# Optimization experiments

Hardware: AMD Instinct MI355X
Metric: run time of the kernel (lower is better)

The kernel has to match this reference:

```python
import jax, jax.numpy as jnp
import numpy as np

N_NODES = 100000

def _sage(x, src, tgt, Wl, bl, Wr):
    # PyG SAGEConv (mean aggr): out = lin_l(mean_{j in N(i)} x_j) + lin_r(x_i)
    msg = x[src]                                             # [E, F] gather
    s = jax.ops.segment_sum(msg, tgt, num_segments=N_NODES)  # [N, F]
    cnt = jax.ops.segment_sum(jnp.ones((src.shape[0], 1), x.dtype), tgt, num_segments=N_NODES)
    agg = s / jnp.maximum(cnt, 1.0)
    return agg @ Wl + bl + x @ Wr


def setup_inputs() -> dict:
    key = jax.random.key(0)
    ks = jax.random.split(key, 16)
    node_dim, edge_dim, hidden = 128, 16, 64
    E = 1000000
    x = jax.random.normal(ks[0], (N_NODES, node_dim), jnp.float32)
    edge_index = jax.random.randint(ks[1], (2, E), 0, N_NODES, jnp.int64)
    edge_attr = jax.random.normal(ks[2], (E, edge_dim), jnp.float32)
    def lin(k, fi, fo, scale=None):
        s = scale if scale is not None else 1.0 / np.sqrt(fi)
        return jax.random.uniform(k, (fi, fo), jnp.float32, -s, s)
    return {
        "x": x, "edge_index": edge_index, "edge_attr": edge_attr,
        # edge MLP: Linear(16,64) -> ReLU -> Linear(64,64)
        "We1": lin(ks[3], edge_dim, hidden), "be1": jnp.zeros((hidden,), jnp.float32),
        "We2": lin(ks[4], hidden, hidden),   "be2": jnp.zeros((hidden,), jnp.float32),
        # SAGEConv 0: lin_l (with bias, on aggregated) + lin_r (no bias, on root)
        "Wl0": lin(ks[5], node_dim, hidden), "bl0": jnp.zeros((hidden,), jnp.float32),
        "Wr0": lin(ks[6], node_dim, hidden),
        # SAGEConv 1
        "Wl1": lin(ks[7], hidden, hidden), "bl1": jnp.zeros((hidden,), jnp.float32),
        "Wr1": lin(ks[8], hidden, hidden),
        # output MLP: Linear(64,64) -> ReLU -> (Dropout eval=id) -> Linear(64,1)
        "Wo1": lin(ks[9], hidden, hidden), "bo1": jnp.zeros((hidden,), jnp.float32),
        "Wo2": lin(ks[10], hidden, 1),     "bo2": jnp.zeros((1,), jnp.float32),
    }


def reference(x, edge_index, edge_attr, We1, be1, We2, be2,
              Wl0, bl0, Wr0, Wl1, bl1, Wr1, Wo1, bo1, Wo2, bo2):
    src, tgt = edge_index[0], edge_index[1]
    # edge MLP (dropout in eval mode = identity)
    ea = jax.nn.relu(edge_attr @ We1 + be1) @ We2 + be2       # [E, H]
    # two SAGE layers with ReLU
    h = jax.nn.relu(_sage(x, src, tgt, Wl0, bl0, Wr0))        # [N, H]
    h = jax.nn.relu(_sage(h, src, tgt, Wl1, bl1, Wr1))        # [N, H]
    # per-edge features: gather both endpoints + edge embedding
    ef = h[src] + h[tgt] + ea                                 # [E, H]
    out = jax.nn.relu(ef @ Wo1 + bo1) @ Wo2 + bo2             # [E, 1]
    return jax.nn.sigmoid(out[:, 0])                          # [E]
```

## Files before the change

kernel.cpp:

```cpp
#include <hip/hip_runtime.h>
#include <math.h>

typedef __attribute__((ext_vector_type(8))) short short8;
typedef __attribute__((ext_vector_type(4))) float f32x4;

static __device__ __forceinline__ unsigned short f2bf(float f) {
  union { float f; unsigned int u; } x; x.f = f;
  unsigned int r = x.u + 0x7fffu + ((x.u >> 16) & 1u);
  return (unsigned short)(r >> 16);
}
static __device__ __forceinline__ float bf2f(unsigned int u) {
  union { unsigned int u; float f; } x; x.u = u << 16; return x.f;
}

__global__ void k_flag(const unsigned int* __restrict__ w, int nSample,
                       unsigned int* __restrict__ flag,
                       int* __restrict__ deg, int padN) {
  int4* d4 = (int4*)deg;
  int n4 = padN >> 2;
  for (int i = blockIdx.x * 256 + threadIdx.x; i < n4; i += gridDim.x * 256)
    d4[i] = make_int4(0, 0, 0, 0);
  if (blockIdx.x != 0) return;
  __shared__ unsigned int red[256];
  unsigned int v = 0;
  for (int i = threadIdx.x; i < nSample; i += 256) v |= w[2 * i + 1];
  red[threadIdx.x] = v;
  __syncthreads();
  for (int s = 128; s > 0; s >>= 1) {
    if (threadIdx.x < s) red[threadIdx.x] |= red[threadIdx.x + s];
    __syncthreads();
  }
  if (threadIdx.x == 0) flag[0] = red[0];
}

__global__ void k_decode(const unsigned int* __restrict__ w,
                         const unsigned int* __restrict__ flag, int E,
                         const float4* __restrict__ ef,
                         uint2* __restrict__ eb,
                         int* __restrict__ src, int* __restrict__ tgt,
                         int* __restrict__ posin, int* __restrict__ deg) {
  int gid = blockIdx.x * 256 + threadIdx.x;
  int stride = gridDim.x * 256;
  for (int i = gid; i < E * 4; i += stride) {
    float4 v = ef[i];
    uint2 pk;
    pk.x = (unsigned int)f2bf(v.x) | ((unsigned int)f2bf(v.y) << 16);
    pk.y = (unsigned int)f2bf(v.z) | ((unsigned int)f2bf(v.w) << 16);
    eb[i] = pk;
  }
  int e = gid;
  if (e >= E) return;
  int s, t;
  if (flag[0]) { s = (int)w[e]; t = (int)w[E + e]; }
  else         { s = (int)w[2 * e]; t = (int)w[2 * (E + e)]; }
  src[e] = s;
  tgt[e] = t;
  posin[e] = atomicAdd(deg + t, 1);
}

__global__ __launch_bounds__(256) void k_scan1(const int* __restrict__ deg,
                                               int* __restrict__ bsum) {
  __shared__ int wsum[4];
  const int tid = threadIdx.x, lane = tid & 63, wid = tid >> 6;
  const int base = blockIdx.x * 2048 + tid * 8;
  int4 v0 = *(const int4*)(deg + base);
  int4 v1 = *(const int4*)(deg + base + 4);
  int s = v0.x + v0.y + v0.z + v0.w + v1.x + v1.y + v1.z + v1.w;
#pragma unroll
  for (int off = 1; off < 64; off <<= 1) s += __shfl_xor(s, off, 64);
  if (lane == 0) wsum[wid] = s;
  __syncthreads();
  if (tid == 0) bsum[blockIdx.x] = wsum[0] + wsum[1] + wsum[2] + wsum[3];
}

__global__ void k_scan2(const int* __restrict__ bsum, int* __restrict__ boff,
                        int nB) {
  int lane = threadIdx.x;
  int v = (lane < nB) ? bsum[lane] : 0;
  int incl = v;
#pragma unroll
  for (int off = 1; off < 64; off <<= 1) {
    int t = __shfl_up(incl, off, 64);
    if (lane >= off) incl += t;
  }
  if (lane < nB) boff[lane] = incl - v;
}

__global__ __launch_bounds__(256) void k_scan3(const int* __restrict__ deg,
                                               const int* __restrict__ boff,
                                               int* __restrict__ rowptr) {
  __shared__ int wsum[4];
  const int tid = threadIdx.x, lane = tid & 63, wid = tid >> 6;
  const int base = blockIdx.x * 2048 + tid * 8;
  int4 v0 = *(const int4*)(deg + base);
  int4 v1 = *(const int4*)(deg + base + 4);
  int e[8] = {v0.x, v0.y, v0.z, v0.w, v1.x, v1.y, v1.z, v1.w};
  int s = e[0] + e[1] + e[2] + e[3] + e[4] + e[5] + e[6] + e[7];
  int incl = s;
#pragma unroll
  for (int off = 1; off < 64; off <<= 1) {
    int t = __shfl_up(incl, off, 64);
    if (lane >= off) incl += t;
  }
  if (lane == 63) wsum[wid] = incl;
  __syncthreads();
  int run = boff[blockIdx.x] + (incl - s);
  for (int w = 0; w < wid; ++w) run += wsum[w];
  int o[8];
#pragma unroll
  for (int i = 0; i < 8; ++i) { o[i] = run; run += e[i]; }
  *(int4*)(rowptr + base) = make_int4(o[0], o[1], o[2], o[3]);
  *(int4*)(rowptr + base + 4) = make_int4(o[4], o[5], o[6], o[7]);
}

__global__ void k_fill(const int* __restrict__ src, const int* __restrict__ tgt,
                       const int* __restrict__ posin,
                       const int* __restrict__ rowptr,
                       int* __restrict__ csrc, int E) {
  int e = blockIdx.x * 256 + threadIdx.x;
  if (e >= E) return;
  csrc[rowptr[tgt[e]] + posin[e]] = src[e];
}

__global__ __launch_bounds__(256) void k_prepall(
    const float* __restrict__ We2, const float* __restrict__ Wo1,
    const float* __restrict__ be2, const float* __restrict__ bo1,
    const float* __restrict__ We1,
    const float* __restrict__ Wl0, const float* __restrict__ Wr0,
    const float* __restrict__ Wl1, const float* __restrict__ Wr1,
    unsigned short* __restrict__ W25T, unsigned short* __restrict__ We1T,
    unsigned short* __restrict__ Wo1T, float* __restrict__ cvec,
    unsigned short* __restrict__ WnT0, unsigned short* __restrict__ WnT1) {
  const int tid = threadIdx.x;
  if (blockIdx.x == 0) {
    __shared__ float sA[4096];
    __shared__ float sB[4096];
    for (int i = tid; i < 1024; i += 256) {
      *(float4*)&sA[i * 4] = *(const float4*)(We2 + i * 4);
      *(float4*)&sB[i * 4] = *(const float4*)(Wo1 + i * 4);
    }
    __syncthreads();
    for (int idx = tid; idx < 4096; idx += 256) {
      int n = idx >> 6, k = idx & 63;
      float s = 0.f;
#pragma unroll 8
      for (int mm = 0; mm < 64; ++mm) s = fmaf(sA[k * 64 + mm], sB[mm * 64 + n], s);
      W25T[idx] = f2bf(s);
      Wo1T[idx] = f2bf(sB[k * 64 + n]);
    }
    for (int idx = tid; idx < 2048; idx += 256) {
      int n = idx >> 5, k = idx & 31;
      We1T[n * 32 + k] = (k < 16) ? f2bf(We1[k * 64 + n]) : (unsigned short)0;
    }
    if (tid < 64) {
      float s = bo1[tid];
#pragma unroll 8
      for (int mm = 0; mm < 64; ++mm) s = fmaf(be2[mm], sB[mm * 64 + tid], s);
      cvec[tid] = s;
    }
  } else if (blockIdx.x <= 64) {
    int idx = (blockIdx.x - 1) * 256 + tid;
    int n = idx >> 7, k = idx & 127;
    float v = (n < 64) ? Wl0[(size_t)k * 64 + n] : Wr0[(size_t)k * 64 + (n - 64)];
    WnT0[idx] = f2bf(v);
  } else {
    int idx = (blockIdx.x - 65) * 256 + tid;
    int n = idx >> 6, k = idx & 63;
    float v = (n < 64) ? Wl1[(size_t)k * 64 + n] : Wr1[(size_t)k * 64 + (n - 64)];
    WnT1[idx] = f2bf(v);
  }
}

template <int K, bool BF16IN, int NTILES>
__global__ __launch_bounds__(256) void k_ngemm(
    const void* __restrict__ Xv, const unsigned short* __restrict__ WnT,
    unsigned short* __restrict__ Y0, unsigned short* __restrict__ Y1, int N) {
  constexpr int STR = K + 8;
  constexpr int NC = K / 32;
  __shared__ unsigned short sX[64 * STR];
  const int tid = threadIdx.x;
  const int wv = tid >> 6, lane = tid & 63;
  const int m = lane & 15, q = lane >> 4;
  const int row0 = blockIdx.x * 64;

  short8 bB[NTILES][NC];
#pragma unroll
  for (int ct = 0; ct < NTILES; ++ct)
#pragma unroll
    for (int c = 0; c < NC; ++c) {
      int n = (NTILES == 2) ? (wv * 32 + ct * 16 + m) : (wv * 16 + m);
      bB[ct][c] = *(const short8*)(WnT + (size_t)n * K + c * 32 + q * 8);
    }

#pragma unroll
  for (int i = 0; i < K / 16; ++i) {
    int f = tid + 256 * i;
    int r = f / (K / 4);
    int c4 = f % (K / 4);
    int rr = row0 + r; if (rr >= N) rr = N - 1;
    uint2 pk;
    if constexpr (BF16IN) {
      pk = *(const uint2*)((const unsigned short*)Xv + (size_t)rr * K + c4 * 4);
    } else {
      float4 v = *(const float4*)((const float*)Xv + (size_t)rr * K + c4 * 4);
      pk.x = (unsigned int)f2bf(v.x) | ((unsigned int)f2bf(v.y) << 16);
      pk.y = (unsigned int)f2bf(v.z) | ((unsigned int)f2bf(v.w) << 16);
    }
    *(uint2*)(sX + r * STR + c4 * 4) = pk;
  }
  __syncthreads();

  f32x4 acc[4][NTILES];
#pragma unroll
  for (int rt = 0; rt < 4; ++rt)
#pragma unroll
    for (int ct = 0; ct < NTILES; ++ct)
#pragma unroll
      for (int r = 0; r < 4; ++r) acc[rt][ct][r] = 0.f;

#pragma unroll
  for (int c = 0; c < NC; ++c) {
    short8 a[4];
#pragma unroll
    for (int rt = 0; rt < 4; ++rt)
      a[rt] = *(const short8*)(sX + (rt * 16 + m) * STR + c * 32 + q * 8);
#pragma unroll
    for (int rt = 0; rt < 4; ++rt)
#pragma unroll
      for (int ct = 0; ct < NTILES; ++ct)
        acc[rt][ct] = __builtin_amdgcn_mfma_f32_16x16x32_bf16(a[rt], bB[ct][c], acc[rt][ct], 0, 0, 0);
  }

#pragma unroll
  for (int rt = 0; rt < 4; ++rt)
#pragma unroll
    for (int ct = 0; ct < NTILES; ++ct) {
      unsigned short* Yw;
      int n;
      if constexpr (NTILES == 2) {
        Yw = (wv < 2) ? Y0 : Y1;
        n = (wv & 1) * 32 + ct * 16 + m;
      } else {
        Yw = Y0;
        n = wv * 16 + m;
      }
#pragma unroll
      for (int reg = 0; reg < 4; ++reg) {
        int row = row0 + rt * 16 + q * 4 + reg;
        if (row < N) Yw[(size_t)row * 64 + n] = f2bf(acc[rt][ct][reg]);
      }
    }
}

__global__ __launch_bounds__(256) void k_agg(
    const unsigned short* __restrict__ Y, const int* __restrict__ rowptr,
    const int* __restrict__ csrc, const float* __restrict__ bias,
    const unsigned short* __restrict__ Yr, unsigned short* __restrict__ H,
    int N) {
  int node = (blockIdx.x * 256 + threadIdx.x) >> 6;
  if (node >= N) return;
  const int lane = threadIdx.x & 63;
  const int c4 = lane & 15, rr = lane >> 4;
  int beg = rowptr[node], end = rowptr[node + 1];
  float a0 = 0.f, a1 = 0.f, a2 = 0.f, a3 = 0.f;
  float b0 = 0.f, b1 = 0.f, b2 = 0.f, b3 = 0.f;
  for (int e = beg; e < end; e += 8) {
    int e0 = e + rr, e1 = e + 4 + rr;
    if (e0 < end) {
      int s = csrc[e0];
      uint2 v = *(const uint2*)(Y + (size_t)s * 64 + c4 * 4);
      a0 += bf2f(v.x & 0xffffu); a1 += bf2f(v.x >> 16);
      a2 += bf2f(v.y & 0xffffu); a3 += bf2f(v.y >> 16);
    }
    if (e1 < end) {
      int s = csrc[e1];
      uint2 v = *(const uint2*)(Y + (size_t)s * 64 + c4 * 4);
      b0 += bf2f(v.x & 0xffffu); b1 += bf2f(v.x >> 16);
      b2 += bf2f(v.y & 0xffffu); b3 += bf2f(v.y >> 16);
    }
  }
  a0 += b0; a1 += b1; a2 += b2; a3 += b3;
#pragma unroll
  for (int msk = 16; msk <= 32; msk <<= 1) {
    a0 += __shfl_xor(a0, msk, 64);
    a1 += __shfl_xor(a1, msk, 64);
    a2 += __shfl_xor(a2, msk, 64);
    a3 += __shfl_xor(a3, msk, 64);
  }
  if (rr == 0) {
    float cdeg = (float)(end - beg);
    if (cdeg < 1.f) cdeg = 1.f;
    float inv = 1.f / cdeg;
    float4 bv = *(const float4*)(bias + c4 * 4);
    uint2 yv = *(const uint2*)(Yr + (size_t)node * 64 + c4 * 4);
    float o0 = fmaxf(a0 * inv + bv.x + bf2f(yv.x & 0xffffu), 0.f);
    float o1 = fmaxf(a1 * inv + bv.y + bf2f(yv.x >> 16), 0.f);
    float o2 = fmaxf(a2 * inv + bv.z + bf2f(yv.y & 0xffffu), 0.f);
    float o3 = fmaxf(a3 * inv + bv.w + bf2f(yv.y >> 16), 0.f);
    uint2 pk;
    pk.x = (unsigned int)f2bf(o0) | ((unsigned int)f2bf(o1) << 16);
    pk.y = (unsigned int)f2bf(o2) | ((unsigned int)f2bf(o3) << 16);
    *(uint2*)(H + (size_t)node * 64 + c4 * 4) = pk;
  }
}

#define T1_STRIDE 72
#define G_STRIDE 68
__global__ __launch_bounds__(256) void k_edge3(
    const unsigned short* __restrict__ EAb, const int* __restrict__ src,
    const int* __restrict__ tgt, const unsigned short* __restrict__ Gb,
    const unsigned short* __restrict__ We1T,
    const unsigned short* __restrict__ W25T,
    const float* __restrict__ cvec, const float* __restrict__ be1,
    const float* __restrict__ Wo2, const float* __restrict__ bo2,
    float* __restrict__ out, int E, int nT, int nWaves) {
  __shared__ unsigned short sT1a[4][16 * T1_STRIDE];
  __shared__ float sGa[4][16 * G_STRIDE];
  const int tid = threadIdx.x;
  const int wid = tid >> 6, lane = tid & 63;
  const int m = lane & 15, q = lane >> 4;
  unsigned short* sT1 = sT1a[wid];
  float* sG = sGa[wid];

  short8 bWe1[4], bW25[4][2];
  float cv[4], wo2v[4], be1v[4];
#pragma unroll
  for (int nt = 0; nt < 4; ++nt) {
    int n = nt * 16 + m;
    bWe1[nt] = *(const short8*)(We1T + n * 32 + q * 8);
    bW25[nt][0] = *(const short8*)(W25T + n * 64 + q * 8);
    bW25[nt][1] = *(const short8*)(W25T + n * 64 + 32 + q * 8);
    cv[nt] = cvec[n];
    wo2v[nt] = Wo2[n];
    be1v[nt] = be1[n];
  }
  const float b_out = bo2[0];
  const short8 zfrag = {};

  int t = blockIdx.x * 4 + wid;
  if (t >= nT) return;
  int il = t * 16 + m; if (il >= E) il = E - 1;
  int my_idx = (lane < 16) ? src[il] : ((lane < 32) ? tgt[il] : 0);

  while (true) {
    const int base = t * 16;
    const int tn = t + nWaves;
    const bool last = (tn >= nT);
    const int tc = last ? t : tn;

    int il_n = tc * 16 + m; if (il_n >= E) il_n = E - 1;
    int idx_n = (lane < 16) ? src[il_n] : ((lane < 32) ? tgt[il_n] : 0);

    int rs[4], rt[4];
#pragma unroll
    for (int r = 0; r < 4; ++r) {
      rs[r] = __shfl(my_idx, q * 4 + r, 64);
      rt[r] = __shfl(my_idx, 16 + q * 4 + r, 64);
    }
    uint2 sv[4], tv[4];
#pragma unroll
    for (int r = 0; r < 4; ++r) {
      sv[r] = *(const uint2*)(Gb + (size_t)rs[r] * 64 + m * 4);
      tv[r] = *(const uint2*)(Gb + (size_t)rt[r] * 64 + m * 4);
    }

    int er = base + m; if (er >= E) er = E - 1;
    short8 aEA = zfrag;
    if (q < 2) aEA = *(const short8*)(EAb + (size_t)er * 16 + (q & 1) * 8);

    f32x4 t1[4];
#pragma unroll
    for (int nt = 0; nt < 4; ++nt) {
      f32x4 cinit; cinit[0] = be1v[nt]; cinit[1] = be1v[nt];
      cinit[2] = be1v[nt]; cinit[3] = be1v[nt];
      t1[nt] = __builtin_amdgcn_mfma_f32_16x16x32_bf16(aEA, bWe1[nt], cinit, 0, 0, 0);
    }
#pragma unroll
    for (int nt = 0; nt < 4; ++nt)
#pragma unroll
      for (int r = 0; r < 4; ++r)
        sT1[(q * 4 + r) * T1_STRIDE + nt * 16 + m] = f2bf(fmaxf(t1[nt][r], 0.f));
    short8 aT0 = *(short8*)(sT1 + m * T1_STRIDE + q * 8);
    short8 aT1 = *(short8*)(sT1 + m * T1_STRIDE + 32 + q * 8);

#pragma unroll
    for (int r = 0; r < 4; ++r) {
      f32x4 g;
      g[0] = bf2f(sv[r].x & 0xffffu) + bf2f(tv[r].x & 0xffffu);
      g[1] = bf2f(sv[r].x >> 16)     + bf2f(tv[r].x >> 16);
      g[2] = bf2f(sv[r].y & 0xffffu) + bf2f(tv[r].y & 0xffffu);
      g[3] = bf2f(sv[r].y >> 16)     + bf2f(tv[r].y >> 16);
      *(f32x4*)(sG + (q * 4 + r) * G_STRIDE + m * 4) = g;
    }

    f32x4 acc[4];
#pragma unroll
    for (int nt = 0; nt < 4; ++nt)
#pragma unroll
      for (int r = 0; r < 4; ++r)
        acc[nt][r] = cv[nt] + sG[(q * 4 + r) * G_STRIDE + nt * 16 + m];
#pragma unroll
    for (int nt = 0; nt < 4; ++nt) {
      acc[nt] = __builtin_amdgcn_mfma_f32_16x16x32_bf16(aT0, bW25[nt][0], acc[nt], 0, 0, 0);
      acc[nt] = __builtin_amdgcn_mfma_f32_16x16x32_bf16(aT1, bW25[nt][1], acc[nt], 0, 0, 0);
    }

    float p[4];
#pragma unroll
    for (int r = 0; r < 4; ++r) {
      p[r] = fmaxf(acc[0][r], 0.f) * wo2v[0] + fmaxf(acc[1][r], 0.f) * wo2v[1] +
             fmaxf(acc[2][r], 0.f) * wo2v[2] + fmaxf(acc[3][r], 0.f) * wo2v[3];
    }
#pragma unroll
    for (int msk = 1; msk <= 8; msk <<= 1) {
#pragma unroll
      for (int r = 0; r < 4; ++r) p[r] += __shfl_xor(p[r], msk, 64);
    }
    if (m == 0) {
#pragma unroll
      for (int r = 0; r < 4; ++r) {
        int row = base + q * 4 + r;
        if (row < E) out[row] = 1.f / (1.f + __expf(-(p[r] + b_out)));
      }
    }

    if (last) break;
    t = tn; my_idx = idx_n;
  }
}

extern "C" void kernel_launch(void* const* d_in, const int* in_sizes, int n_in,
                              void* d_out, int out_size, void* d_ws, size_t ws_size,
                              hipStream_t stream) {
  const float* x     = (const float*)d_in[0];
  const unsigned int* eidx = (const unsigned int*)d_in[1];
  const float* eattr = (const float*)d_in[2];
  const float* We1 = (const float*)d_in[3];
  const float* be1 = (const float*)d_in[4];
  const float* We2 = (const float*)d_in[5];
  const float* be2 = (const float*)d_in[6];
  const float* Wl0 = (const float*)d_in[7];
  const float* bl0 = (const float*)d_in[8];
  const float* Wr0 = (const float*)d_in[9];
  const float* Wl1 = (const float*)d_in[10];
  const float* bl1 = (const float*)d_in[11];
  const float* Wr1 = (const float*)d_in[12];
  const float* Wo1 = (const float*)d_in[13];
  const float* bo1 = (const float*)d_in[14];
  const float* Wo2 = (const float*)d_in[15];
  const float* bo2 = (const float*)d_in[16];

  const int N = in_sizes[0] / 128;
  const int E = in_sizes[2] / 16;
  const int padN = (N + 2047) & ~2047;
  const int nB = padN / 2048;
  float* out = (float*)d_out;

  char* ws = (char*)d_ws;
  size_t off = 0;
  auto alloc = [&](size_t bytes) {
    char* p = ws + off;
    off += (bytes + 255) & ~(size_t)255;
    return p;
  };
  unsigned int* flag = (unsigned int*)alloc(256);
  int* src    = (int*)alloc((size_t)E * 4);
  int* tgt    = (int*)alloc((size_t)E * 4);
  int* posin  = (int*)alloc((size_t)E * 4);
  int* deg    = (int*)alloc((size_t)padN * 4);
  int* rowptr = (int*)alloc((size_t)(padN + 64) * 4);
  int* bsum   = (int*)alloc(64 * 4);
  int* boff   = (int*)alloc(64 * 4);
  int* csrc   = (int*)alloc((size_t)E * 4);
  unsigned short* EAb = (unsigned short*)alloc((size_t)E * 16 * 2);
  unsigned short* Hb = (unsigned short*)alloc((size_t)N * 64 * 2);
  unsigned short* Yl = (unsigned short*)alloc((size_t)N * 64 * 2);
  unsigned short* Yr = (unsigned short*)alloc((size_t)N * 64 * 2);
  unsigned short* Gb = (unsigned short*)alloc((size_t)N * 64 * 2);
  unsigned short* W25T = (unsigned short*)alloc(64 * 64 * 2);
  unsigned short* We1T = (unsigned short*)alloc(64 * 32 * 2);
  unsigned short* Wo1T = (unsigned short*)alloc(64 * 64 * 2);
  unsigned short* WnT0 = (unsigned short*)alloc(128 * 128 * 2);
  unsigned short* WnT1 = (unsigned short*)alloc(128 * 64 * 2);
  float* cvec = (float*)alloc(64 * 4);
  (void)ws_size; (void)n_in; (void)out_size;

  k_flag<<<64, 256, 0, stream>>>(eidx, 8192, flag, deg, padN);
  k_decode<<<(E + 255) / 256, 256, 0, stream>>>(
      eidx, flag, E, (const float4*)eattr, (uint2*)EAb, src, tgt, posin, deg);
  k_scan1<<<nB, 256, 0, stream>>>(deg, bsum);
  k_scan2<<<1, 64, 0, stream>>>(bsum, boff, nB);
  k_scan3<<<nB, 256, 0, stream>>>(deg, boff, rowptr);
  k_fill<<<(E + 255) / 256, 256, 0, stream>>>(src, tgt, posin, rowptr, csrc, E);
  k_prepall<<<97, 256, 0, stream>>>(We2, Wo1, be2, bo1, We1, Wl0, Wr0, Wl1, Wr1,
                                    W25T, We1T, Wo1T, cvec, WnT0, WnT1);

  const int gB = (N + 63) / 64;
  k_ngemm<128, false, 2><<<gB, 256, 0, stream>>>(x, WnT0, Yl, Yr, N);
  k_agg<<<(N + 3) / 4, 256, 0, stream>>>(Yl, rowptr, csrc, bl0, Yr, Hb, N);

  k_ngemm<64, true, 2><<<gB, 256, 0, stream>>>(Hb, WnT1, Yl, Yr, N);
  k_agg<<<(N + 3) / 4, 256, 0, stream>>>(Yl, rowptr, csrc, bl1, Yr, Hb, N);

  k_ngemm<64, true, 1><<<gB, 256, 0, stream>>>(Hb, Wo1T, Gb, nullptr, N);

  const int nT = (E + 15) / 16;
  const int blocks = 3072;
  k_edge3<<<blocks, 256, 0, stream>>>(EAb, src, tgt, Gb, We1T, W25T, cvec,
                                      be1, Wo2, bo2, out, E, nT, blocks * 4);
}
```

Baseline: 456.4 us.

## Merge independent launches into horizontally fused multi-role kernels

Independent stages now share a launch through block-index role dispatch. Edge decoding is merged with weight preparation, the CSR fill with the first node GEMM, and the edge-attribute bf16 conversion with the first aggregation. This removes several kernel launches and lets bandwidth-bound and gather-bound work overlap on the GPU. The W25T prep now reads We2 from global memory instead of shared memory. Mixed roles inside one grid can unbalance scheduling, and the fused kernels may use more registers or LDS.

```diff
diff --git a/kernel.cpp b/kernel.cpp
--- a/kernel.cpp
+++ b/kernel.cpp
@@ -33,29 +33,66 @@
   if (threadIdx.x == 0) flag[0] = red[0];
 }
 
-__global__ void k_decode(const unsigned int* __restrict__ w,
-                         const unsigned int* __restrict__ flag, int E,
-                         const float4* __restrict__ ef,
-                         uint2* __restrict__ eb,
-                         int* __restrict__ src, int* __restrict__ tgt,
-                         int* __restrict__ posin, int* __restrict__ deg) {
-  int gid = blockIdx.x * 256 + threadIdx.x;
-  int stride = gridDim.x * 256;
-  for (int i = gid; i < E * 4; i += stride) {
-    float4 v = ef[i];
-    uint2 pk;
-    pk.x = (unsigned int)f2bf(v.x) | ((unsigned int)f2bf(v.y) << 16);
-    pk.y = (unsigned int)f2bf(v.z) | ((unsigned int)f2bf(v.w) << 16);
-    eb[i] = pk;
-  }
-  int e = gid;
-  if (e >= E) return;
-  int s, t;
-  if (flag[0]) { s = (int)w[e]; t = (int)w[E + e]; }
-  else         { s = (int)w[2 * e]; t = (int)w[2 * (E + e)]; }
-  src[e] = s;
-  tgt[e] = t;
-  posin[e] = atomicAdd(deg + t, 1);
+__global__ __launch_bounds__(256) void k_mega1(
+    const unsigned int* __restrict__ w, const unsigned int* __restrict__ flag,
+    int E, int nDec,
+    int* __restrict__ src, int* __restrict__ tgt,
+    int* __restrict__ posin, int* __restrict__ deg,
+    const float* __restrict__ We2, const float* __restrict__ Wo1,
+    const float* __restrict__ be2, const float* __restrict__ bo1,
+    const float* __restrict__ We1,
+    const float* __restrict__ Wl0, const float* __restrict__ Wr0,
+    const float* __restrict__ Wl1, const float* __restrict__ Wr1,
+    unsigned short* __restrict__ W25T, unsigned short* __restrict__ We1T,
+    unsigned short* __restrict__ Wo1T, float* __restrict__ cvec,
+    unsigned short* __restrict__ WnT0, unsigned short* __restrict__ WnT1) {
+  __shared__ float sB[4096];
+  const int tid = threadIdx.x;
+  if (blockIdx.x < nDec) {
+    int e = blockIdx.x * 256 + tid;
+    if (e >= E) return;
+    int s, t;
+    if (flag[0]) { s = (int)w[e]; t = (int)w[E + e]; }
+    else         { s = (int)w[2 * e]; t = (int)w[2 * (E + e)]; }
+    src[e] = s;
+    tgt[e] = t;
+    posin[e] = atomicAdd(deg + t, 1);
+    return;
+  }
+  const int b = blockIdx.x - nDec;
+  if (b == 0) {
+    for (int i = tid; i < 1024; i += 256)
+      *(float4*)&sB[i * 4] = *(const float4*)(Wo1 + i * 4);
+    __syncthreads();
+    for (int idx = tid; idx < 4096; idx += 256) {
+      int k = idx >> 6, n = idx & 63;
+      float s = 0.f;
+#pragma unroll 8
+      for (int mm = 0; mm < 64; ++mm) s = fmaf(We2[k * 64 + mm], sB[mm * 64 + n], s);
+      W25T[n * 64 + k] = f2bf(s);
+      Wo1T[n * 64 + k] = f2bf(sB[k * 64 + n]);
+    }
+    for (int idx = tid; idx < 2048; idx += 256) {
+      int n = idx >> 5, k = idx & 31;
+      We1T[n * 32 + k] = (k < 16) ? f2bf(We1[k * 64 + n]) : (unsigned short)0;
+    }
+    if (tid < 64) {
+      float s = bo1[tid];
+#pragma unroll 8
+      for (int mm = 0; mm < 64; ++mm) s = fmaf(be2[mm], sB[mm * 64 + tid], s);
+      cvec[tid] = s;
+    }
+  } else if (b <= 64) {
+    int idx = (b - 1) * 256 + tid;
+    int n = idx >> 7, k = idx & 127;
+    float v = (n < 64) ? Wl0[(size_t)k * 64 + n] : Wr0[(size_t)k * 64 + (n - 64)];
+    WnT0[idx] = f2bf(v);
+  } else {
+    int idx = (b - 65) * 256 + tid;
+    int n = idx >> 6, k = idx & 63;
+    float v = (n < 64) ? Wl1[(size_t)k * 64 + n] : Wr1[(size_t)k * 64 + (n - 64)];
+    WnT1[idx] = f2bf(v);
+  }
 }
 
 __global__ __launch_bounds__(256) void k_scan1(const int* __restrict__ deg,
@@ -113,75 +150,18 @@
   *(int4*)(rowptr + base + 4) = make_int4(o[4], o[5], o[6], o[7]);
 }
 
-__global__ void k_fill(const int* __restrict__ src, const int* __restrict__ tgt,
-                       const int* __restrict__ posin,
-                       const int* __restrict__ rowptr,
-                       int* __restrict__ csrc, int E) {
-  int e = blockIdx.x * 256 + threadIdx.x;
-  if (e >= E) return;
-  csrc[rowptr[tgt[e]] + posin[e]] = src[e];
-}
-
-__global__ __launch_bounds__(256) void k_prepall(
-    const float* __restrict__ We2, const float* __restrict__ Wo1,
-    const float* __restrict__ be2, const float* __restrict__ bo1,
-    const float* __restrict__ We1,
-    const float* __restrict__ Wl0, const float* __restrict__ Wr0,
-    const float* __restrict__ Wl1, const float* __restrict__ Wr1,
-    unsigned short* __restrict__ W25T, unsigned short* __restrict__ We1T,
-    unsigned short* __restrict__ Wo1T, float* __restrict__ cvec,
-    unsigned short* __restrict__ WnT0, unsigned short* __restrict__ WnT1) {
-  const int tid = threadIdx.x;
-  if (blockIdx.x == 0) {
-    __shared__ float sA[4096];
-    __shared__ float sB[4096];
-    for (int i = tid; i < 1024; i += 256) {
-      *(float4*)&sA[i * 4] = *(const float4*)(We2 + i * 4);
-      *(float4*)&sB[i * 4] = *(const float4*)(Wo1 + i * 4);
-    }
-    __syncthreads();
-    for (int idx = tid; idx < 4096; idx += 256) {
-      int n = idx >> 6, k = idx & 63;
-      float s = 0.f;
-#pragma unroll 8
-      for (int mm = 0; mm < 64; ++mm) s = fmaf(sA[k * 64 + mm], sB[mm * 64 + n], s);
-      W25T[idx] = f2bf(s);
-      Wo1T[idx] = f2bf(sB[k * 64 + n]);
-    }
-    for (int idx = tid; idx < 2048; idx += 256) {
-      int n = idx >> 5, k = idx & 31;
-      We1T[n * 32 + k] = (k < 16) ? f2bf(We1[k * 64 + n]) : (unsigned short)0;
-    }
-    if (tid < 64) {
-      float s = bo1[tid];
-#pragma unroll 8
-      for (int mm = 0; mm < 64; ++mm) s = fmaf(be2[mm], sB[mm * 64 + tid], s);
-      cvec[tid] = s;
-    }
-  } else if (blockIdx.x <= 64) {
-    int idx = (blockIdx.x - 1) * 256 + tid;
-    int n = idx >> 7, k = idx & 127;
-    float v = (n < 64) ? Wl0[(size_t)k * 64 + n] : Wr0[(size_t)k * 64 + (n - 64)];
-    WnT0[idx] = f2bf(v);
-  } else {
-    int idx = (blockIdx.x - 65) * 256 + tid;
-    int n = idx >> 6, k = idx & 63;
-    float v = (n < 64) ? Wl1[(size_t)k * 64 + n] : Wr1[(size_t)k * 64 + (n - 64)];
-    WnT1[idx] = f2bf(v);
-  }
-}
-
 template <int K, bool BF16IN, int NTILES>
-__global__ __launch_bounds__(256) void k_ngemm(
+__device__ __forceinline__ void ngemm_body(
     const void* __restrict__ Xv, const unsigned short* __restrict__ WnT,
-    unsigned short* __restrict__ Y0, unsigned short* __restrict__ Y1, int N) {
+    unsigned short* __restrict__ Y0, unsigned short* __restrict__ Y1,
+    int N, int blk) {
   constexpr int STR = K + 8;
   constexpr int NC = K / 32;
   __shared__ unsigned short sX[64 * STR];
   const int tid = threadIdx.x;
   const int wv = tid >> 6, lane = tid & 63;
   const int m = lane & 15, q = lane >> 4;
-  const int row0 = blockIdx.x * 64;
+  const int row0 = blk * 64;
 
   short8 bB[NTILES][NC];
 #pragma unroll
@@ -252,12 +232,35 @@
     }
 }
 
-__global__ __launch_bounds__(256) void k_agg(
+template <int K, bool BF16IN, int NTILES>
+__global__ __launch_bounds__(256) void k_ngemm(
+    const void* __restrict__ Xv, const unsigned short* __restrict__ WnT,
+    unsigned short* __restrict__ Y0, unsigned short* __restrict__ Y1, int N) {
+  ngemm_body<K, BF16IN, NTILES>(Xv, WnT, Y0, Y1, N, blockIdx.x);
+}
+
+__global__ __launch_bounds__(256) void k_mega2(
+    const void* __restrict__ Xv, const unsigned short* __restrict__ WnT,
+    unsigned short* __restrict__ Y0, unsigned short* __restrict__ Y1, int N,
+    int gB,
+    const int* __restrict__ src, const int* __restrict__ tgt,
+    const int* __restrict__ posin, const int* __restrict__ rowptr,
+    int* __restrict__ csrc, int E) {
+  if (blockIdx.x < gB) {
+    ngemm_body<128, false, 2>(Xv, WnT, Y0, Y1, N, blockIdx.x);
+  } else {
+    int e = (blockIdx.x - gB) * 256 + threadIdx.x;
+    if (e >= E) return;
+    csrc[rowptr[tgt[e]] + posin[e]] = src[e];
+  }
+}
+
+__device__ __forceinline__ void agg_body(
     const unsigned short* __restrict__ Y, const int* __restrict__ rowptr,
     const int* __restrict__ csrc, const float* __restrict__ bias,
     const unsigned short* __restrict__ Yr, unsigned short* __restrict__ H,
-    int N) {
-  int node = (blockIdx.x * 256 + threadIdx.x) >> 6;
+    int N, int blk) {
+  int node = (blk * 256 + threadIdx.x) >> 6;
   if (node >= N) return;
   const int lane = threadIdx.x & 63;
   const int c4 = lane & 15, rr = lane >> 4;
@@ -301,6 +304,35 @@
     pk.x = (unsigned int)f2bf(o0) | ((unsigned int)f2bf(o1) << 16);
     pk.y = (unsigned int)f2bf(o2) | ((unsigned int)f2bf(o3) << 16);
     *(uint2*)(H + (size_t)node * 64 + c4 * 4) = pk;
+  }
+}
+
+__global__ __launch_bounds__(256) void k_agg(
+    const unsigned short* __restrict__ Y, const int* __restrict__ rowptr,
+    const int* __restrict__ csrc, const float* __restrict__ bias,
+    const unsigned short* __restrict__ Yr, unsigned short* __restrict__ H,
+    int N) {
+  agg_body(Y, rowptr, csrc, bias, Yr, H, N, blockIdx.x);
+}
+
+__global__ __launch_bounds__(256) void k_aggc(
+    const unsigned short* __restrict__ Y, const int* __restrict__ rowptr,
+    const int* __restrict__ csrc, const float* __restrict__ bias,
+    const unsigned short* __restrict__ Yr, unsigned short* __restrict__ H,
+    int N, int aggB,
+    const float4* __restrict__ ef, uint2* __restrict__ eb, int nItems,
+    int nConvThreads) {
+  if (blockIdx.x < aggB) {
+    agg_body(Y, rowptr, csrc, bias, Yr, H, N, blockIdx.x);
+  } else {
+    int gid = (blockIdx.x - aggB) * 256 + threadIdx.x;
+    for (int i = gid; i < nItems; i += nConvThreads) {
+      float4 v = ef[i];
+      uint2 pk;
+      pk.x = (unsigned int)f2bf(v.x) | ((unsigned int)f2bf(v.y) << 16);
+      pk.y = (unsigned int)f2bf(v.z) | ((unsigned int)f2bf(v.w) << 16);
+      eb[i] = pk;
+    }
   }
 }
 
@@ -486,21 +518,29 @@
   (void)ws_size; (void)n_in; (void)out_size;
 
   k_flag<<<64, 256, 0, stream>>>(eidx, 8192, flag, deg, padN);
-  k_decode<<<(E + 255) / 256, 256, 0, stream>>>(
-      eidx, flag, E, (const float4*)eattr, (uint2*)EAb, src, tgt, posin, deg);
+
+  const int nDec = (E + 255) / 256;
+  k_mega1<<<nDec + 97, 256, 0, stream>>>(
+      eidx, flag, E, nDec, src, tgt, posin, deg,
+      We2, Wo1, be2, bo1, We1, Wl0, Wr0, Wl1, Wr1,
+      W25T, We1T, Wo1T, cvec, WnT0, WnT1);
+
   k_scan1<<<nB, 256, 0, stream>>>(deg, bsum);
   k_scan2<<<1, 64, 0, stream>>>(bsum, boff, nB);
   k_scan3<<<nB, 256, 0, stream>>>(deg, boff, rowptr);
-  k_fill<<<(E + 255) / 256, 256, 0, stream>>>(src, tgt, posin, rowptr, csrc, E);
-  k_prepall<<<97, 256, 0, stream>>>(We2, Wo1, be2, bo1, We1, Wl0, Wr0, Wl1, Wr1,
-                                    W25T, We1T, Wo1T, cvec, WnT0, WnT1);
 
   const int gB = (N + 63) / 64;
-  k_ngemm<128, false, 2><<<gB, 256, 0, stream>>>(x, WnT0, Yl, Yr, N);
-  k_agg<<<(N + 3) / 4, 256, 0, stream>>>(Yl, rowptr, csrc, bl0, Yr, Hb, N);
+  k_mega2<<<gB + nDec, 256, 0, stream>>>(x, WnT0, Yl, Yr, N, gB,
+                                         src, tgt, posin, rowptr, csrc, E);
+
+  const int aggB = (N + 3) / 4;
+  const int convB = 2048;
+  k_aggc<<<aggB + convB, 256, 0, stream>>>(Yl, rowptr, csrc, bl0, Yr, Hb, N,
+                                           aggB, (const float4*)eattr,
+                                           (uint2*)EAb, E * 4, convB * 256);
 
   k_ngemm<64, true, 2><<<gB, 256, 0, stream>>>(Hb, WnT1, Yl, Yr, N);
-  k_agg<<<(N + 3) / 4, 256, 0, stream>>>(Yl, rowptr, csrc, bl1, Yr, Hb, N);
+  k_agg<<<aggB, 256, 0, stream>>>(Yl, rowptr, csrc, bl1, Yr, Hb, N);
 
   k_ngemm<64, true, 1><<<gB, 256, 0, stream>>>(Hb, Wo1T, Gb, nullptr, N);
 
```

After: 446.2 us. 1.02x faster.

## Fuse edge decode, weight prep, first node GEMM and edge-attr conversion into one kernel

Applied to the files above, without the earlier changes.

Merges edge index decoding with degree atomics, weight transposition and packing, the first-layer node GEMM, and the edge-attribute bf16 conversion into a single heterogeneous launch. Block roles are interleaved so decode blocks are spread among the work blocks. The first GEMM now reads fp32 weights directly and converts them inline, which drops the separate prep kernel and the WnT0 buffer. This removes several launches and their serialization so independent memory-bound work can overlap, at the cost of redundant per-block weight conversion and a bulkier kernel with shared-memory sizing tied to the largest role.

```diff
diff --git a/kernel.cpp b/kernel.cpp
--- a/kernel.cpp
+++ b/kernel.cpp
@@ -33,163 +33,37 @@
   if (threadIdx.x == 0) flag[0] = red[0];
 }
 
-__global__ void k_decode(const unsigned int* __restrict__ w,
-                         const unsigned int* __restrict__ flag, int E,
-                         const float4* __restrict__ ef,
-                         uint2* __restrict__ eb,
-                         int* __restrict__ src, int* __restrict__ tgt,
-                         int* __restrict__ posin, int* __restrict__ deg) {
-  int gid = blockIdx.x * 256 + threadIdx.x;
-  int stride = gridDim.x * 256;
-  for (int i = gid; i < E * 4; i += stride) {
-    float4 v = ef[i];
-    uint2 pk;
-    pk.x = (unsigned int)f2bf(v.x) | ((unsigned int)f2bf(v.y) << 16);
-    pk.y = (unsigned int)f2bf(v.z) | ((unsigned int)f2bf(v.w) << 16);
-    eb[i] = pk;
-  }
-  int e = gid;
-  if (e >= E) return;
-  int s, t;
-  if (flag[0]) { s = (int)w[e]; t = (int)w[E + e]; }
-  else         { s = (int)w[2 * e]; t = (int)w[2 * (E + e)]; }
-  src[e] = s;
-  tgt[e] = t;
-  posin[e] = atomicAdd(deg + t, 1);
-}
-
-__global__ __launch_bounds__(256) void k_scan1(const int* __restrict__ deg,
-                                               int* __restrict__ bsum) {
-  __shared__ int wsum[4];
-  const int tid = threadIdx.x, lane = tid & 63, wid = tid >> 6;
-  const int base = blockIdx.x * 2048 + tid * 8;
-  int4 v0 = *(const int4*)(deg + base);
-  int4 v1 = *(const int4*)(deg + base + 4);
-  int s = v0.x + v0.y + v0.z + v0.w + v1.x + v1.y + v1.z + v1.w;
-#pragma unroll
-  for (int off = 1; off < 64; off <<= 1) s += __shfl_xor(s, off, 64);
-  if (lane == 0) wsum[wid] = s;
-  __syncthreads();
-  if (tid == 0) bsum[blockIdx.x] = wsum[0] + wsum[1] + wsum[2] + wsum[3];
-}
-
-__global__ void k_scan2(const int* __restrict__ bsum, int* __restrict__ boff,
-                        int nB) {
-  int lane = threadIdx.x;
-  int v = (lane < nB) ? bsum[lane] : 0;
-  int incl = v;
-#pragma unroll
-  for (int off = 1; off < 64; off <<= 1) {
-    int t = __shfl_up(incl, off, 64);
-    if (lane >= off) incl += t;
-  }
-  if (lane < nB) boff[lane] = incl - v;
-}
-
-__global__ __launch_bounds__(256) void k_scan3(const int* __restrict__ deg,
-                                               const int* __restrict__ boff,
-                                               int* __restrict__ rowptr) {
-  __shared__ int wsum[4];
-  const int tid = threadIdx.x, lane = tid & 63, wid = tid >> 6;
-  const int base = blockIdx.x * 2048 + tid * 8;
-  int4 v0 = *(const int4*)(deg + base);
-  int4 v1 = *(const int4*)(deg + base + 4);
-  int e[8] = {v0.x, v0.y, v0.z, v0.w, v1.x, v1.y, v1.z, v1.w};
-  int s = e[0] + e[1] + e[2] + e[3] + e[4] + e[5] + e[6] + e[7];
-  int incl = s;
-#pragma unroll
-  for (int off = 1; off < 64; off <<= 1) {
-    int t = __shfl_up(incl, off, 64);
-    if (lane >= off) incl += t;
-  }
-  if (lane == 63) wsum[wid] = incl;
-  __syncthreads();
-  int run = boff[blockIdx.x] + (incl - s);
-  for (int w = 0; w < wid; ++w) run += wsum[w];
-  int o[8];
-#pragma unroll
-  for (int i = 0; i < 8; ++i) { o[i] = run; run += e[i]; }
-  *(int4*)(rowptr + base) = make_int4(o[0], o[1], o[2], o[3]);
-  *(int4*)(rowptr + base + 4) = make_int4(o[4], o[5], o[6], o[7]);
-}
-
-__global__ void k_fill(const int* __restrict__ src, const int* __restrict__ tgt,
-                       const int* __restrict__ posin,
-                       const int* __restrict__ rowptr,
-                       int* __restrict__ csrc, int E) {
-  int e = blockIdx.x * 256 + threadIdx.x;
-  if (e >= E) return;
-  csrc[rowptr[tgt[e]] + posin[e]] = src[e];
-}
-
-__global__ __launch_bounds__(256) void k_prepall(
-    const float* __restrict__ We2, const float* __restrict__ Wo1,
-    const float* __restrict__ be2, const float* __restrict__ bo1,
-    const float* __restrict__ We1,
-    const float* __restrict__ Wl0, const float* __restrict__ Wr0,
-    const float* __restrict__ Wl1, const float* __restrict__ Wr1,
-    unsigned short* __restrict__ W25T, unsigned short* __restrict__ We1T,
-    unsigned short* __restrict__ Wo1T, float* __restrict__ cvec,
-    unsigned short* __restrict__ WnT0, unsigned short* __restrict__ WnT1) {
-  const int tid = threadIdx.x;
-  if (blockIdx.x == 0) {
-    __shared__ float sA[4096];
-    __shared__ float sB[4096];
-    for (int i = tid; i < 1024; i += 256) {
-      *(float4*)&sA[i * 4] = *(const float4*)(We2 + i * 4);
-      *(float4*)&sB[i * 4] = *(const float4*)(Wo1 + i * 4);
-    }
-    __syncthreads();
-    for (int idx = tid; idx < 4096; idx += 256) {
-      int n = idx >> 6, k = idx & 63;
-      float s = 0.f;
-#pragma unroll 8
-      for (int mm = 0; mm < 64; ++mm) s = fmaf(sA[k * 64 + mm], sB[mm * 64 + n], s);
-      W25T[idx] = f2bf(s);
-      Wo1T[idx] = f2bf(sB[k * 64 + n]);
-    }
-    for (int idx = tid; idx < 2048; idx += 256) {
-      int n = idx >> 5, k = idx & 31;
-      We1T[n * 32 + k] = (k < 16) ? f2bf(We1[k * 64 + n]) : (unsigned short)0;
-    }
-    if (tid < 64) {
-      float s = bo1[tid];
-#pragma unroll 8
-      for (int mm = 0; mm < 64; ++mm) s = fmaf(be2[mm], sB[mm * 64 + tid], s);
-      cvec[tid] = s;
-    }
-  } else if (blockIdx.x <= 64) {
-    int idx = (blockIdx.x - 1) * 256 + tid;
-    int n = idx >> 7, k = idx & 127;
-    float v = (n < 64) ? Wl0[(size_t)k * 64 + n] : Wr0[(size_t)k * 64 + (n - 64)];
-    WnT0[idx] = f2bf(v);
-  } else {
-    int idx = (blockIdx.x - 65) * 256 + tid;
-    int n = idx >> 6, k = idx & 63;
-    float v = (n < 64) ? Wl1[(size_t)k * 64 + n] : Wr1[(size_t)k * 64 + (n - 64)];
-    WnT1[idx] = f2bf(v);
-  }
-}
-
-template <int K, bool BF16IN, int NTILES>
-__global__ __launch_bounds__(256) void k_ngemm(
+template <int K, bool BF16IN, int NTILES, bool INLINEW>
+__device__ __forceinline__ void ngemm_body(
     const void* __restrict__ Xv, const unsigned short* __restrict__ WnT,
-    unsigned short* __restrict__ Y0, unsigned short* __restrict__ Y1, int N) {
+    const float* __restrict__ W0f, const float* __restrict__ W1f,
+    unsigned short* __restrict__ Y0, unsigned short* __restrict__ Y1,
+    int N, int blk, unsigned short* __restrict__ sX) {
   constexpr int STR = K + 8;
   constexpr int NC = K / 32;
-  __shared__ unsigned short sX[64 * STR];
   const int tid = threadIdx.x;
   const int wv = tid >> 6, lane = tid & 63;
   const int m = lane & 15, q = lane >> 4;
-  const int row0 = blockIdx.x * 64;
+  const int row0 = blk * 64;
 
   short8 bB[NTILES][NC];
 #pragma unroll
   for (int ct = 0; ct < NTILES; ++ct)
 #pragma unroll
     for (int c = 0; c < NC; ++c) {
-      int n = (NTILES == 2) ? (wv * 32 + ct * 16 + m) : (wv * 16 + m);
-      bB[ct][c] = *(const short8*)(WnT + (size_t)n * K + c * 32 + q * 8);
+      if constexpr (INLINEW) {
+        int n = (NTILES == 2) ? (wv * 32 + ct * 16 + m) : (wv * 16 + m);
+        const float* Wf = (n < 64) ? W0f : W1f;
+        int nn = n & 63;
+        union { short8 s; unsigned short h[8]; } ub;
+#pragma unroll
+        for (int j = 0; j < 8; ++j)
+          ub.h[j] = f2bf(Wf[(size_t)(c * 32 + q * 8 + j) * 64 + nn]);
+        bB[ct][c] = ub.s;
+      } else {
+        int n = (NTILES == 2) ? (wv * 32 + ct * 16 + m) : (wv * 16 + m);
+        bB[ct][c] = *(const short8*)(WnT + (size_t)n * K + c * 32 + q * 8);
+      }
     }
 
 #pragma unroll
@@ -250,6 +124,157 @@
         if (row < N) Yw[(size_t)row * 64 + n] = f2bf(acc[rt][ct][reg]);
       }
     }
+}
+
+template <int K, bool BF16IN, int NTILES>
+__global__ __launch_bounds__(256) void k_ngemm(
+    const void* __restrict__ Xv, const unsigned short* __restrict__ WnT,
+    unsigned short* __restrict__ Y0, unsigned short* __restrict__ Y1, int N) {
+  __shared__ __align__(16) unsigned short sX[64 * (K + 8)];
+  ngemm_body<K, BF16IN, NTILES, false>(Xv, WnT, nullptr, nullptr, Y0, Y1, N,
+                                       blockIdx.x, sX);
+}
+
+__global__ __launch_bounds__(256) void k_mega1(
+    const unsigned int* __restrict__ w, const unsigned int* __restrict__ flag,
+    int E, int nDec, int nWork, int gB, int nConvThreads,
+    int* __restrict__ src, int* __restrict__ tgt,
+    int* __restrict__ posin, int* __restrict__ deg,
+    const float* __restrict__ x, unsigned short* __restrict__ Yl,
+    unsigned short* __restrict__ Yr, int N,
+    const float* __restrict__ We2, const float* __restrict__ Wo1,
+    const float* __restrict__ be2, const float* __restrict__ bo1,
+    const float* __restrict__ We1,
+    const float* __restrict__ Wl0, const float* __restrict__ Wr0,
+    const float* __restrict__ Wl1, const float* __restrict__ Wr1,
+    unsigned short* __restrict__ W25T, unsigned short* __restrict__ We1T,
+    unsigned short* __restrict__ Wo1T, float* __restrict__ cvec,
+    unsigned short* __restrict__ WnT1,
+    const float4* __restrict__ ef, uint2* __restrict__ eb) {
+  __shared__ __align__(16) char smem[64 * 136 * 2];
+  const int tid = threadIdx.x;
+  const int tot = nDec + nWork;
+  const int di  = (int)(((long long)blockIdx.x * nDec) / tot);
+  const int di1 = (int)(((long long)(blockIdx.x + 1) * nDec) / tot);
+
+  if (di1 > di) {
+    int e = di * 256 + tid;
+    if (e >= E) return;
+    int s, t;
+    if (flag[0]) { s = (int)w[e]; t = (int)w[E + e]; }
+    else         { s = (int)w[2 * e]; t = (int)w[2 * (E + e)]; }
+    src[e] = s;
+    tgt[e] = t;
+    posin[e] = atomicAdd(deg + t, 1);
+    return;
+  }
+  const int wi = blockIdx.x - di;
+  if (wi == 0) {
+    float* sB = (float*)smem;
+    for (int i = tid; i < 1024; i += 256)
+      *(float4*)&sB[i * 4] = *(const float4*)(Wo1 + i * 4);
+    __syncthreads();
+    for (int idx = tid; idx < 4096; idx += 256) {
+      int k = idx >> 6, n = idx & 63;
+      float s = 0.f;
+#pragma unroll 8
+      for (int mm = 0; mm < 64; ++mm) s = fmaf(We2[k * 64 + mm], sB[mm * 64 + n], s);
+      W25T[n * 64 + k] = f2bf(s);
+      Wo1T[n * 64 + k] = f2bf(sB[k * 64 + n]);
+    }
+    for (int idx = tid; idx < 2048; idx += 256) {
+      int n = idx >> 5, k = idx & 31;
+      We1T[n * 32 + k] = (k < 16) ? f2bf(We1[k * 64 + n]) : (unsigned short)0;
+    }
+    if (tid < 64) {
+      float s = bo1[tid];
+#pragma unroll 8
+      for (int mm = 0; mm < 64; ++mm) s = fmaf(be2[mm], sB[mm * 64 + tid], s);
+      cvec[tid] = s;
+    }
+  } else if (wi <= 32) {
+    int idx = (wi - 1) * 256 + tid;
+    int n = idx >> 6, k = idx & 63;
+    float v = (n < 64) ? Wl1[(size_t)k * 64 + n] : Wr1[(size_t)k * 64 + (n - 64)];
+    WnT1[idx] = f2bf(v);
+  } else if (wi < 33 + gB) {
+    ngemm_body<128, false, 2, true>(x, nullptr, Wl0, Wr0, Yl, Yr, N,
+                                    wi - 33, (unsigned short*)smem);
+  } else {
+    int gid = (wi - 33 - gB) * 256 + tid;
+    int nItems = E * 4;
+    for (int i = gid; i < nItems; i += nConvThreads) {
+      float4 v = ef[i];
+      uint2 pk;
+      pk.x = (unsigned int)f2bf(v.x) | ((unsigned int)f2bf(v.y) << 16);
+      pk.y = (unsigned int)f2bf(v.z) | ((unsigned int)f2bf(v.w) << 16);
+      eb[i] = pk;
+    }
+  }
+}
+
+__global__ __launch_bounds__(256) void k_scan1(const int* __restrict__ deg,
+                                               int* __restrict__ bsum) {
+  __shared__ int wsum[4];
+  const int tid = threadIdx.x, lane = tid & 63, wid = tid >> 6;
+  const int base = blockIdx.x * 2048 + tid * 8;
+  int4 v0 = *(const int4*)(deg + base);
+  int4 v1 = *(const int4*)(deg + base + 4);
+  int s = v0.x + v0.y + v0.z + v0.w + v1.x + v1.y + v1.z + v1.w;
+#pragma unroll
+  for (int off = 1; off < 64; off <<= 1) s += __shfl_xor(s, off, 64);
+  if (lane == 0) wsum[wid] = s;
+  __syncthreads();
+  if (tid == 0) bsum[blockIdx.x] = wsum[0] + wsum[1] + wsum[2] + wsum[3];
+}
+
+__global__ void k_scan2(const int* __restrict__ bsum, int* __restrict__ boff,
+                        int nB) {
+  int lane = threadIdx.x;
+  int v = (lane < nB) ? bsum[lane] : 0;
+  int incl = v;
+#pragma unroll
+  for (int off = 1; off < 64; off <<= 1) {
+    int t = __shfl_up(incl, off, 64);
+    if (lane >= off) incl += t;
+  }
+  if (lane < nB) boff[lane] = incl - v;
+}
+
+__global__ __launch_bounds__(256) void k_scan3(const int* __restrict__ deg,
+                                               const int* __restrict__ boff,
+                                               int* __restrict__ rowptr) {
+  __shared__ int wsum[4];
+  const int tid = threadIdx.x, lane = tid & 63, wid = tid >> 6;
+  const int base = blockIdx.x * 2048 + tid * 8;
+  int4 v0 = *(const int4*)(deg + base);
+  int4 v1 = *(const int4*)(deg + base + 4);
+  int e[8] = {v0.x, v0.y, v0.z, v0.w, v1.x, v1.y, v1.z, v1.w};
+  int s = e[0] + e[1] + e[2] + e[3] + e[4] + e[5] + e[6] + e[7];
+  int incl = s;
+#pragma unroll
+  for (int off = 1; off < 64; off <<= 1) {
+    int t = __shfl_up(incl, off, 64);
+    if (lane >= off) incl += t;
+  }
+  if (lane == 63) wsum[wid] = incl;
+  __syncthreads();
+  int run = boff[blockIdx.x] + (incl - s);
+  for (int w = 0; w < wid; ++w) run += wsum[w];
+  int o[8];
+#pragma unroll
+  for (int i = 0; i < 8; ++i) { o[i] = run; run += e[i]; }
+  *(int4*)(rowptr + base) = make_int4(o[0], o[1], o[2], o[3]);
+  *(int4*)(rowptr + base + 4) = make_int4(o[4], o[5], o[6], o[7]);
+}
+
+__global__ void k_fill(const int* __restrict__ src, const int* __restrict__ tgt,
+                       const int* __restrict__ posin,
+                       const int* __restrict__ rowptr,
+                       int* __restrict__ csrc, int E) {
+  int e = blockIdx.x * 256 + threadIdx.x;
+  if (e >= E) return;
+  csrc[rowptr[tgt[e]] + posin[e]] = src[e];
 }
 
 __global__ __launch_bounds__(256) void k_agg(
@@ -480,27 +505,34 @@
   unsigned short* W25T = (unsigned short*)alloc(64 * 64 * 2);
   unsigned short* We1T = (unsigned short*)alloc(64 * 32 * 2);
   unsigned short* Wo1T = (unsigned short*)alloc(64 * 64 * 2);
-  unsigned short* WnT0 = (unsigned short*)alloc(128 * 128 * 2);
   unsigned short* WnT1 = (unsigned short*)alloc(128 * 64 * 2);
   float* cvec = (float*)alloc(64 * 4);
   (void)ws_size; (void)n_in; (void)out_size;
 
   k_flag<<<64, 256, 0, stream>>>(eidx, 8192, flag, deg, padN);
-  k_decode<<<(E + 255) / 256, 256, 0, stream>>>(
-      eidx, flag, E, (const float4*)eattr, (uint2*)EAb, src, tgt, posin, deg);
+
+  const int nDec = (E + 255) / 256;
+  const int gB = (N + 63) / 64;
+  const int convB = 1024;
+  const int nWork = 33 + gB + convB;
+  k_mega1<<<nDec + nWork, 256, 0, stream>>>(
+      eidx, flag, E, nDec, nWork, gB, convB * 256,
+      src, tgt, posin, deg,
+      x, Yl, Yr, N,
+      We2, Wo1, be2, bo1, We1, Wl0, Wr0, Wl1, Wr1,
+      W25T, We1T, Wo1T, cvec, WnT1,
+      (const float4*)eattr, (uint2*)EAb);
+
   k_scan1<<<nB, 256, 0, stream>>>(deg, bsum);
   k_scan2<<<1, 64, 0, stream>>>(bsum, boff, nB);
   k_scan3<<<nB, 256, 0, stream>>>(deg, boff, rowptr);
-  k_fill<<<(E + 255) / 256, 256, 0, stream>>>(src, tgt, posin, rowptr, csrc, E);
-  k_prepall<<<97, 256, 0, stream>>>(We2, Wo1, be2, bo1, We1, Wl0, Wr0, Wl1, Wr1,
-                                    W25T, We1T, Wo1T, cvec, WnT0, WnT1);
-
-  const int gB = (N + 63) / 64;
-  k_ngemm<128, false, 2><<<gB, 256, 0, stream>>>(x, WnT0, Yl, Yr, N);
-  k_agg<<<(N + 3) / 4, 256, 0, stream>>>(Yl, rowptr, csrc, bl0, Yr, Hb, N);
+  k_fill<<<nDec, 256, 0, stream>>>(src, tgt, posin, rowptr, csrc, E);
+
+  const int aggB = (N + 3) / 4;
+  k_agg<<<aggB, 256, 0, stream>>>(Yl, rowptr, csrc, bl0, Yr, Hb, N);
 
   k_ngemm<64, true, 2><<<gB, 256, 0, stream>>>(Hb, WnT1, Yl, Yr, N);
-  k_agg<<<(N + 3) / 4, 256, 0, stream>>>(Yl, rowptr, csrc, bl1, Yr, Hb, N);
+  k_agg<<<aggB, 256, 0, stream>>>(Yl, rowptr, csrc, bl1, Yr, Hb, N);
 
   k_ngemm<64, true, 1><<<gB, 256, 0, stream>>>(Hb, Wo1T, Gb, nullptr, N);
 
```

New measurement: 412.8 us. 9.6% less time.
